# Optimization experiments

Measured on AMD Instinct MI355X. Metric: run time of the kernel, lower is better.

## Reference

```python
import jax, jax.numpy as jnp
import numpy as np

B, T, H = 4, 4096, 1024


def setup_inputs() -> dict:
    key = jax.random.key(0)
    ks = jax.random.split(key, 10)
    W_STD = 0.02  # small init keeps the WKV denominator well-conditioned
    inp = {
        "x": jax.random.normal(ks[0], (B, T, H), dtype=jnp.float32),
        "time_decay": jnp.exp(-jax.random.uniform(ks[1], (H,), minval=0.5, maxval=1.5)),
        "time_mix_key": jax.random.uniform(ks[2], (H,)),
        "time_mix_value": jax.random.uniform(ks[3], (H,)),
        "time_mix_receptance": jax.random.uniform(ks[4], (H,)),
        "W_receptance": jax.random.normal(ks[5], (H, H)) * W_STD,
        "W_key": jax.random.normal(ks[6], (H, H)) * W_STD,
        "W_value": jax.random.normal(ks[7], (H, H)) * W_STD,
        "W_out": jax.random.normal(ks[8], (H, H)) * W_STD,
        "b_out": jax.random.normal(ks[9], (H,)) * W_STD,
    }
    return inp


def reference(x, time_decay, time_mix_key, time_mix_value, time_mix_receptance,
              W_receptance, W_key, W_value, W_out, b_out):
    # time_shift: shifted[:, t] = x[:, t-1], shifted[:, 0] = 0
    shifted = jnp.pad(x, ((0, 0), (1, 0), (0, 0)))[:, :-1]
    xs = x + shifted  # original applies SAME mix to x and shifted
    k = (xs * time_mix_key) @ W_key.T          # [B,T,H]
    v = (xs * time_mix_value) @ W_value.T      # [B,T,H]
    r = jax.nn.sigmoid((xs * time_mix_receptance) @ W_receptance.T)

    def step(carry, kv):
        num, den = carry                       # [B,H] each
        ck, cv = kv                            # [B,H]
        out = (num + time_decay * ck * den) / (den + time_decay * ck)
        ek = jnp.exp(ck)
        return (time_decay * num + ek * cv, time_decay * den + ek), out

    init = (jnp.ones_like(k[:, 0]), jnp.ones_like(k[:, 0]))
    kT = jnp.swapaxes(k, 0, 1)  # [T,B,H]
    vT = jnp.swapaxes(v, 0, 1)
    _, outT = jax.lax.scan(step, init, (kT, vT))
    out = jnp.swapaxes(outT, 0, 1)             # [B,T,H]
    return (r * out) @ W_out.T + b_out
```

## Files before the change

### kernel.cpp

```cpp
#include <hip/hip_runtime.h>

#define H_DIM 1024
#define T_DIM 4096
#define B_DIM 4
#define M_DIM (B_DIM * T_DIM)
#define SCAN_C 64
#define SCAN_W 48

typedef __attribute__((ext_vector_type(8))) short short8;
typedef __attribute__((ext_vector_type(4))) float f32x4;
typedef _Float16 half8 __attribute__((ext_vector_type(8)));

__device__ __forceinline__ unsigned short f2h(float f) {
  _Float16 h = (_Float16)f;
  return __builtin_bit_cast(unsigned short, h);
}
__device__ __forceinline__ float h2f(unsigned short u) {
  return (float)__builtin_bit_cast(_Float16, u);
}

__device__ __forceinline__ double fast_exp64(double x) {
  const double L2E = 1.4426950408889634074;
  const double LN2 = 0.69314718055994530942;
  double z = x * L2E;
  double n = rint(z);
  double y = (z - n) * LN2;
  double p = 2.7557319223985890653e-6;
  p = fma(p, y, 2.4801587301587301566e-5);
  p = fma(p, y, 1.9841269841269841253e-4);
  p = fma(p, y, 1.3888888888888889419e-3);
  p = fma(p, y, 8.3333333333333332177e-3);
  p = fma(p, y, 4.1666666666666664354e-2);
  p = fma(p, y, 1.6666666666666665741e-1);
  p = fma(p, y, 0.5);
  p = fma(p, y, 1.0);
  p = fma(p, y, 1.0);
  long long bits = ((long long)(1023 + (int)n)) << 52;
  return p * __longlong_as_double(bits);
}

__global__ void xs_split_kernel(const float* __restrict__ x,
                                unsigned short* __restrict__ xs1,
                                unsigned short* __restrict__ xs2,
                                int n4) {
  int i = blockIdx.x * blockDim.x + threadIdx.x;
  const int HV = H_DIM / 4;
  if (i >= n4) return;
  int m = i / HV;
  int t = m & (T_DIM - 1);
  float4 cur = reinterpret_cast<const float4*>(x)[i];
  float4 prev = make_float4(0.f, 0.f, 0.f, 0.f);
  if (t > 0) prev = reinterpret_cast<const float4*>(x)[i - HV];
  float s[4] = {cur.x + prev.x, cur.y + prev.y, cur.z + prev.z, cur.w + prev.w};
  unsigned short a1[4], a2[4];
#pragma unroll
  for (int q = 0; q < 4; ++q) {
    unsigned short h1 = f2h(s[q]);
    a1[q] = h1;
    a2[q] = f2h((s[q] - h2f(h1)) * 2048.0f);
  }
  reinterpret_cast<ushort4*>(xs1)[i] = make_ushort4(a1[0], a1[1], a1[2], a1[3]);
  reinterpret_cast<ushort4*>(xs2)[i] = make_ushort4(a2[0], a2[1], a2[2], a2[3]);
}

__global__ void wprep_kernel(const float* __restrict__ Wrec, const float* __restrict__ Wkey,
                             const float* __restrict__ Wval, const float* __restrict__ Wout,
                             const float* __restrict__ tmk, const float* __restrict__ tmv,
                             const float* __restrict__ tmr,
                             unsigned short* __restrict__ WK1H, unsigned short* __restrict__ WK2H,
                             unsigned short* __restrict__ WVRH,
                             unsigned short* __restrict__ WOH) {
  int i = blockIdx.x * blockDim.x + threadIdx.x;
  if (i >= H_DIM * H_DIM) return;
  int j = i & (H_DIM - 1);
  float wk = Wkey[i] * tmk[j];
  unsigned short k1 = f2h(wk);
  WK1H[i] = k1;
  WK2H[i] = f2h((wk - h2f(k1)) * 2048.0f);
  WVRH[i] = f2h(Wval[i] * tmv[j]);
  WVRH[H_DIM * H_DIM + i] = f2h(Wrec[i] * tmr[j]);
  WOH[i] = f2h(Wout[i]);
}

#define GBAR() do { asm volatile("" ::: "memory"); __builtin_amdgcn_sched_barrier(0); \
                    __builtin_amdgcn_s_barrier(); \
                    __builtin_amdgcn_sched_barrier(0); asm volatile("" ::: "memory"); } while (0)
#define WAIT_VM6() asm volatile("s_waitcnt vmcnt(6)" ::: "memory")
#define WAIT_VM0() asm volatile("s_waitcnt vmcnt(0)" ::: "memory")

__device__ __forceinline__ f32x4 mma_h(short8 a, short8 b, f32x4 c) {
  return __builtin_amdgcn_mfma_f32_16x16x32_f16(
      __builtin_bit_cast(half8, a), __builtin_bit_cast(half8, b), c, 0, 0, 0);
}
__device__ __forceinline__ f32x4 mma_hh(half8 a, short8 b, f32x4 c) {
  return __builtin_amdgcn_mfma_f32_16x16x32_f16(a, __builtin_bit_cast(half8, b), c, 0, 0, 0);
}

__device__ __forceinline__ void stage_A32(const unsigned short* base, int rowoff, int kt,
                                          unsigned sbase, int wid, int lane,
                                          unsigned char* smem) {
#pragma unroll
  for (int i = 0; i < 2; ++i) {
    int row = wid * 32 + i * 16 + (lane >> 2);
    int col8 = (lane & 3) ^ ((row >> 1) & 3);
    const unsigned short* src = base + (size_t)(rowoff + row) * 1024 + kt * 32 + col8 * 8;
    __builtin_amdgcn_global_load_lds(
        (const __attribute__((address_space(1))) void*)src,
        (__attribute__((address_space(3))) void*)(smem + sbase + wid * 2048 + i * 1024), 16, 0, 0);
  }
}
__device__ __forceinline__ void stage_B32(const unsigned short* base, int coloff, int kt,
                                          unsigned sbase, int wid, int lane,
                                          unsigned char* smem) {
  int row = wid * 16 + (lane >> 2);
  int col8 = (lane & 3) ^ ((row >> 1) & 3);
  const unsigned short* src = base + (size_t)(coloff + row) * 1024 + kt * 32 + col8 * 8;
  __builtin_amdgcn_global_load_lds(
      (const __attribute__((address_space(1))) void*)src,
      (__attribute__((address_space(3))) void*)(smem + sbase + wid * 1024), 16, 0, 0);
}
__device__ __forceinline__ short8 frag_ld2(const unsigned char* smem, unsigned rbase,
                                           int row, int kg) {
  return *reinterpret_cast<const short8*>(smem + rbase + row * 64 + ((kg ^ ((row >> 1) & 3)) * 16));
}

__global__ __launch_bounds__(512, 2) void gemm_k_kernel(
    const unsigned short* __restrict__ A1, const unsigned short* __restrict__ A2,
    const unsigned short* __restrict__ B1, const unsigned short* __restrict__ B2,
    float* __restrict__ C) {
  __shared__ __attribute__((aligned(16))) unsigned char smem[147456];
  const int tid = threadIdx.x;
  const int wid = tid >> 6;
  const int lane = tid & 63;
  const int wm = wid >> 2;
  const int wn = wid & 3;
  const int frow = lane & 15;
  const int kg = lane >> 4;
  const int nwg = gridDim.x * gridDim.y;
  const int wg = blockIdx.y * gridDim.x + blockIdx.x;
  const int swz = (wg & 7) * (nwg >> 3) + (wg >> 3);
  const int brow = (swz / gridDim.x) << 8;
  const int bcol = (swz % gridDim.x) << 7;

  f32x4 acc0[8][2], acc1[8][2];
#pragma unroll
  for (int f = 0; f < 8; ++f)
#pragma unroll
    for (int c = 0; c < 2; ++c) {
      acc0[f][c] = (f32x4){0.f, 0.f, 0.f, 0.f};
      acc1[f][c] = (f32x4){0.f, 0.f, 0.f, 0.f};
    }

  const int NT = 32;
#pragma unroll
  for (int t0 = 0; t0 < 2; ++t0) {
    unsigned sb = t0 * 49152u;
    stage_A32(A1, brow, t0, sb + 0u, wid, lane, smem);
    stage_A32(A2, brow, t0, sb + 16384u, wid, lane, smem);
    stage_B32(B1, bcol, t0, sb + 32768u, wid, lane, smem);
    stage_B32(B2, bcol, t0, sb + 40960u, wid, lane, smem);
  }
  WAIT_VM6();
  GBAR();

  for (int t = 0; t < NT; ++t) {
    unsigned sb = (unsigned)(t % 3) * 49152u;
    unsigned st = (unsigned)((t + 2) % 3) * 49152u;
    const bool stg = (t + 2 < NT);
    short8 a1[8], a2[8], b1[2], b2[2];
#pragma unroll
    for (int f = 0; f < 8; ++f) a1[f] = frag_ld2(smem, sb, wm * 128 + f * 16 + frow, kg);
#pragma unroll
    for (int c = 0; c < 2; ++c) b1[c] = frag_ld2(smem, sb + 32768u, wn * 32 + c * 16 + frow, kg);
    if (stg) stage_A32(A1, brow, t + 2, st + 0u, wid, lane, smem);
    GBAR();
    __builtin_amdgcn_s_setprio(1);
#pragma unroll
    for (int f = 0; f < 8; ++f)
#pragma unroll
      for (int c = 0; c < 2; ++c)
        acc0[f][c] = mma_h(a1[f], b1[c], acc0[f][c]);
    __builtin_amdgcn_s_setprio(0);
    GBAR();
#pragma unroll
    for (int c = 0; c < 2; ++c) b2[c] = frag_ld2(smem, sb + 40960u, wn * 32 + c * 16 + frow, kg);
    if (stg) stage_A32(A2, brow, t + 2, st + 16384u, wid, lane, smem);
    GBAR();
    __builtin_amdgcn_s_setprio(1);
#pragma unroll
    for (int f = 0; f < 8; ++f)
#pragma unroll
      for (int c = 0; c < 2; ++c)
        acc1[f][c] = mma_h(a1[f], b2[c], acc1[f][c]);
    __builtin_amdgcn_s_setprio(0);
    GBAR();
#pragma unroll
    for (int f = 0; f < 8; ++f) a2[f] = frag_ld2(smem, sb + 16384u, wm * 128 + f * 16 + frow, kg);
    if (stg) {
      stage_B32(B1, bcol, t + 2, st + 32768u, wid, lane, smem);
      stage_B32(B2, bcol, t + 2, st + 40960u, wid, lane, smem);
    }
    GBAR();
    __builtin_amdgcn_s_setprio(1);
#pragma unroll
    for (int f = 0; f < 8; ++f)
#pragma unroll
      for (int c = 0; c < 2; ++c)
        acc1[f][c] = mma_h(a2[f], b1[c], acc1[f][c]);
    __builtin_amdgcn_s_setprio(0);
    GBAR();
    WAIT_VM6();
    GBAR();
    __builtin_amdgcn_s_setprio(1);
#pragma unroll
    for (int f = 0; f < 8; ++f) {
      half8 ad = __builtin_bit_cast(half8, a2[f]) * (_Float16)0.00048828125f;
#pragma unroll
      for (int c = 0; c < 2; ++c)
        acc1[f][c] = mma_hh(ad, b2[c], acc1[f][c]);
    }
    __builtin_amdgcn_s_setprio(0);
    GBAR();
  }
  WAIT_VM0();

#pragma unroll
  for (int f = 0; f < 8; ++f) {
    int r0 = brow + wm * 128 + f * 16 + kg * 4;
#pragma unroll
    for (int c = 0; c < 2; ++c) {
      int cc = bcol + wn * 32 + c * 16 + frow;
#pragma unroll
      for (int q = 0; q < 4; ++q)
        C[(size_t)(r0 + q) * H_DIM + cc] =
            fmaf(0.00048828125f, acc1[f][c][q], acc0[f][c][q]);
    }
  }
}

struct GemmPasses {
  const unsigned short* A[2];
  const unsigned short* B[2];
  int n;
};

__device__ __forceinline__ void stage_half(const unsigned short* base, int rowoff,
                                           int ktp, int kk, int slot,
                                           int wid, int lane, unsigned char* smem) {
#pragma unroll
  for (int i = 0; i < 2; ++i) {
    int row = wid * 32 + i * 16 + (lane >> 2);
    int kcol8 = (lane & 3) ^ ((row >> 1) & 3);
    const unsigned short* src = base + (size_t)(rowoff + row) * 1024
                                + ktp * 64 + kk * 32 + kcol8 * 8;
    unsigned int doff = (unsigned int)(slot * 16384 + wid * 2048 + i * 1024);
    __builtin_amdgcn_global_load_lds(
        (const __attribute__((address_space(1))) void*)src,
        (__attribute__((address_space(3))) void*)(smem + doff), 16, 0, 0);
  }
}
__device__ __forceinline__ short8 frag_ld(const unsigned char* smem, int slot, int row, int kg) {
  int byte = slot * 16384 + row * 64 + ((kg ^ ((row >> 1) & 3)) * 16);
  return *reinterpret_cast<const short8*>(smem + byte);
}

__global__ __launch_bounds__(512, 2) void gemm256_kernel(GemmPasses P, void* __restrict__ Cout,
                                                         int N, int NT,
                                                         const float* __restrict__ bias,
                                                         int omode) {
  __shared__ __attribute__((aligned(16))) unsigned char smem[131072];
  const int tid = threadIdx.x;
  const int wid = tid >> 6;
  const int lane = tid & 63;
  const int wm = wid >> 2;
  const int wn = wid & 3;
  const int frow = lane & 15;
  const int kg = lane >> 4;
  const int nwg = gridDim.x * gridDim.y;
  const int wg = blockIdx.y * gridDim.x + blockIdx.x;
  const int swz = (wg & 7) * (nwg >> 3) + (wg >> 3);
  const int brow = (swz / gridDim.x) << 8;
  const int bcol = (swz % gridDim.x) << 8;

  f32x4 acc[8][4];
#pragma unroll
  for (int f = 0; f < 8; ++f)
#pragma unroll
    for (int c = 0; c < 4; ++c)
      acc[f][c] = (f32x4){0.f, 0.f, 0.f, 0.f};

  const unsigned short* Ag = P.A[0];
  const unsigned short* Bg = P.B[0];
  stage_half(Ag, brow, 0, 0, 0, wid, lane, smem);
  stage_half(Bg, bcol, 0, 0, 1, wid, lane, smem);
  stage_half(Ag, brow, 0, 1, 2, wid, lane, smem);
  stage_half(Bg, bcol, 0, 1, 3, wid, lane, smem);
  stage_half(Ag, brow, 1, 0, 4, wid, lane, smem);
  stage_half(Bg, bcol, 1, 0, 5, wid, lane, smem);
  stage_half(Ag, brow, 1, 1, 6, wid, lane, smem);
  WAIT_VM6();
  GBAR();

  for (int t = 0; t < NT; ++t) {
    const int cur4 = (t & 1) * 4;
    const int nxt4 = cur4 ^ 4;
    const unsigned short* Agp = P.A[(t >> 4) >= P.n ? P.n - 1 : (t >> 4)];
    const unsigned short* Bgp = P.B[(t >> 4) >= P.n ? P.n - 1 : (t >> 4)];
    short8 a[4], b[4];
#pragma unroll
    for (int f = 0; f < 4; ++f) a[f] = frag_ld(smem, cur4 + 0, wm * 128 + f * 16 + frow, kg);
#pragma unroll
    for (int c = 0; c < 4; ++c) b[c] = frag_ld(smem, cur4 + 1, wn * 64 + c * 16 + frow, kg);
    if (t + 1 < NT) {
      int ts = t + 1;
      stage_half(P.B[(ts >> 4)], bcol, ts & 15, 1, nxt4 + 3, wid, lane, smem);
    }
    GBAR();
    __builtin_amdgcn_s_setprio(1);
#pragma unroll
    for (int f = 0; f < 4; ++f)
#pragma unroll
      for (int c = 0; c < 4; ++c)
        acc[f][c] = mma_h(a[f], b[c], acc[f][c]);
    __builtin_amdgcn_s_setprio(0);
    GBAR();
#pragma unroll
    for (int f = 0; f < 4; ++f) a[f] = frag_ld(smem, cur4 + 0, wm * 128 + (f + 4) * 16 + frow, kg);
    if (t + 2 < NT) {
      int ts = t + 2;
      stage_half(P.A[(ts >> 4)], brow, ts & 15, 0, cur4 + 0, wid, lane, smem);
    }
    GBAR();
    __builtin_amdgcn_s_setprio(1);
#pragma unroll
    for (int f = 0; f < 4; ++f)
#pragma unroll
      for (int c = 0; c < 4; ++c)
        acc[f + 4][c] = mma_h(a[f], b[c], acc[f + 4][c]);
    __builtin_amdgcn_s_setprio(0);
    GBAR();
#pragma unroll
    for (int f = 0; f < 4; ++f) a[f] = frag_ld(smem, cur4 + 2, wm * 128 + f * 16 + frow, kg);
#pragma unroll
    for (int c = 0; c < 4; ++c) b[c] = frag_ld(smem, cur4 + 3, wn * 64 + c * 16 + frow, kg);
    if (t + 2 < NT) {
      int ts = t + 2;
      stage_half(P.B[(ts >> 4)], bcol, ts & 15, 0, cur4 + 1, wid, lane, smem);
    }
    GBAR();
    __builtin_amdgcn_s_setprio(1);
#pragma unroll
    for (int f = 0; f < 4; ++f)
#pragma unroll
      for (int c = 0; c < 4; ++c)
        acc[f][c] = mma_h(a[f], b[c], acc[f][c]);
    __builtin_amdgcn_s_setprio(0);
    GBAR();
#pragma unroll
    for (int f = 0; f < 4; ++f) a[f] = frag_ld(smem, cur4 + 2, wm * 128 + (f + 4) * 16 + frow, kg);
    if (t + 2 < NT) {
      int ts = t + 2;
      stage_half(P.A[(ts >> 4)], brow, ts & 15, 1, cur4 + 2, wid, lane, smem);
    }
    WAIT_VM6();
    GBAR();
    __builtin_amdgcn_s_setprio(1);
#pragma unroll
    for (int f = 0; f < 4; ++f)
#pragma unroll
      for (int c = 0; c < 4; ++c)
        acc[f + 4][c] = mma_h(a[f], b[c], acc[f + 4][c]);
    __builtin_amdgcn_s_setprio(0);
    GBAR();
  }
  WAIT_VM0();

#pragma unroll
  for (int f = 0; f < 8; ++f) {
    int r0 = brow + wm * 128 + f * 16 + kg * 4;
#pragma unroll
    for (int c = 0; c < 4; ++c) {
      int cc = bcol + wn * 64 + c * 16 + frow;
      if (omode == 0) {
        float bb = bias ? bias[cc] : 0.f;
        float* C = (float*)Cout;
#pragma unroll
        for (int q = 0; q < 4; ++q)
          C[(size_t)(r0 + q) * N + cc] = acc[f][c][q] + bb;
      } else {
        unsigned short* C = (unsigned short*)Cout;
#pragma unroll
        for (int q = 0; q < 4; ++q)
          C[(size_t)(r0 + q) * N + cc] = f2h(acc[f][c][q]);
      }
    }
  }
}

__global__ void wkv_scan_kernel(const float* __restrict__ kbuf,
                                const unsigned short* __restrict__ vrbuf,
                                const float* __restrict__ tdec,
                                unsigned short* __restrict__ rwh) {
  const int h = blockIdx.x * 64 + threadIdx.x;
  const int chunk = blockIdx.y;
  const int b = blockIdx.z;
  const int t0 = chunk * SCAN_C;
  const int tstart = (chunk == 0) ? 0 : (t0 - SCAN_W);
  const int tend = t0 + SCAN_C;
  double num, den;
  if (chunk == 0) { num = 1.0; den = 1.0; } else { num = 0.0; den = 0.0; }
  const double w = (double)tdec[h];
  size_t ik = ((size_t)b * T_DIM + tstart) * H_DIM + h;
  size_t iv = ((size_t)b * T_DIM + tstart) * 2048 + h;
  float kc = kbuf[ik];
  unsigned short vc = vrbuf[iv];
  unsigned short rc = vrbuf[iv + 1024];
  for (int t = tstart; t < tend; ++t) {
    int adv = (t + 1 < tend) ? 1 : 0;
    float kn = kbuf[ik + adv * H_DIM];
    unsigned short vn = vrbuf[iv + adv * 2048];
    unsigned short rn = vrbuf[iv + adv * 2048 + 1024];
    double ck = (double)kc;
    if (t >= t0) {
      double p = w * ck;
      double A = fma(p, den, num);
      double Bd = den + p;
      float outf = (float)A / (float)Bd;
      float rr = 1.0f / (1.0f + __expf(-h2f(rc)));
      rwh[ik] = f2h(rr * outf);
    }
    double ek = fast_exp64(ck);
    num = fma(w, num, ek * (double)h2f(vc));
    den = fma(w, den, ek);
    kc = kn; vc = vn; rc = rn;
    ik += H_DIM; iv += 2048;
  }
}

static inline void run_gemm256(const GemmPasses& P, void* C, int Mrows, int N,
                               const float* bias, int omode, hipStream_t stream) {
  gemm256_kernel<<<dim3(N / 256, Mrows / 256), dim3(512), 0, stream>>>(
      P, C, N, P.n * 16, bias, omode);
}

extern "C" void kernel_launch(void* const* d_in, const int* in_sizes, int n_in,
                              void* d_out, int out_size, void* d_ws, size_t ws_size,
                              hipStream_t stream) {
  const float* x    = (const float*)d_in[0];
  const float* tdec = (const float*)d_in[1];
  const float* tmk  = (const float*)d_in[2];
  const float* tmv  = (const float*)d_in[3];
  const float* tmr  = (const float*)d_in[4];
  const float* Wrec = (const float*)d_in[5];
  const float* Wkey = (const float*)d_in[6];
  const float* Wval = (const float*)d_in[7];
  const float* Wout = (const float*)d_in[8];
  const float* bout = (const float*)d_in[9];
  float* out = (float*)d_out;
  unsigned char* ws = (unsigned char*)d_ws;

  const size_t W2 = (size_t)H_DIM * H_DIM * 2;
  const size_t BF_FULL = (size_t)M_DIM * H_DIM * 2;
  const size_t NEED = 2 * BF_FULL + 2 * BF_FULL + 5 * W2;
  if (ws_size < NEED) return;

  size_t off = 0;
  unsigned short* XS1H = (unsigned short*)(ws + off); off += BF_FULL;
  unsigned short* XS2H = (unsigned short*)(ws + off); off += BF_FULL;
  unsigned short* VR   = (unsigned short*)(ws + off); off += 2 * BF_FULL;
  unsigned short* WK1H = (unsigned short*)(ws + off); off += W2;
  unsigned short* WK2H = (unsigned short*)(ws + off); off += W2;
  unsigned short* WVRH = (unsigned short*)(ws + off); off += 2 * W2;
  unsigned short* WOH  = (unsigned short*)(ws + off); off += W2;

  wprep_kernel<<<dim3(H_DIM * H_DIM / 256), dim3(256), 0, stream>>>(
      Wrec, Wkey, Wval, Wout, tmk, tmv, tmr, WK1H, WK2H, WVRH, WOH);

  int n4 = M_DIM * (H_DIM / 4);
  xs_split_kernel<<<dim3(n4 / 256), dim3(256), 0, stream>>>(x, XS1H, XS2H, n4);

  GemmPasses Pvr;
  Pvr.n = 1;
  Pvr.A[0] = XS1H; Pvr.B[0] = WVRH; Pvr.A[1] = XS1H; Pvr.B[1] = WVRH;
  run_gemm256(Pvr, VR, M_DIM, 2 * H_DIM, nullptr, 2, stream);

  gemm_k_kernel<<<dim3(H_DIM / 128, M_DIM / 256), dim3(512), 0, stream>>>(
      XS1H, XS2H, WK1H, WK2H, out);

  unsigned short* RWH = XS1H;
  wkv_scan_kernel<<<dim3(H_DIM / 64, T_DIM / SCAN_C, B_DIM), dim3(64), 0, stream>>>(
      out, VR, tdec, RWH);

  GemmPasses Po;
  Po.n = 1;
  Po.A[0] = RWH; Po.B[0] = WOH; Po.A[1] = RWH; Po.B[1] = WOH;
  run_gemm256(Po, out, M_DIM, H_DIM, bout, 0, stream);
}
```

Baseline: 338.2 us.

## Merge K and VR projection GEMMs into one launch and retile K GEMM

```diff
diff --git a/kernel.cpp b/kernel.cpp
--- a/kernel.cpp
+++ b/kernel.cpp
@@ -96,9 +96,19 @@
   return __builtin_amdgcn_mfma_f32_16x16x32_f16(a, __builtin_bit_cast(half8, b), c, 0, 0, 0);
 }
 
-__device__ __forceinline__ void stage_A32(const unsigned short* base, int rowoff, int kt,
-                                          unsigned sbase, int wid, int lane,
-                                          unsigned char* smem) {
+__device__ __forceinline__ void stage_r128(const unsigned short* base, int rowoff, int kt,
+                                           unsigned dst, int wid, int lane,
+                                           unsigned char* smem) {
+  int row = wid * 16 + (lane >> 2);
+  int col8 = (lane & 3) ^ ((row >> 1) & 3);
+  const unsigned short* src = base + (size_t)(rowoff + row) * 1024 + kt * 32 + col8 * 8;
+  __builtin_amdgcn_global_load_lds(
+      (const __attribute__((address_space(1))) void*)src,
+      (__attribute__((address_space(3))) void*)(smem + dst + wid * 1024), 16, 0, 0);
+}
+__device__ __forceinline__ void stage_r256(const unsigned short* base, int rowoff, int kt,
+                                           unsigned dst, int wid, int lane,
+                                           unsigned char* smem) {
 #pragma unroll
   for (int i = 0; i < 2; ++i) {
     int row = wid * 32 + i * 16 + (lane >> 2);
@@ -106,29 +116,19 @@
     const unsigned short* src = base + (size_t)(rowoff + row) * 1024 + kt * 32 + col8 * 8;
     __builtin_amdgcn_global_load_lds(
         (const __attribute__((address_space(1))) void*)src,
-        (__attribute__((address_space(3))) void*)(smem + sbase + wid * 2048 + i * 1024), 16, 0, 0);
-  }
-}
-__device__ __forceinline__ void stage_B32(const unsigned short* base, int coloff, int kt,
-                                          unsigned sbase, int wid, int lane,
-                                          unsigned char* smem) {
-  int row = wid * 16 + (lane >> 2);
-  int col8 = (lane & 3) ^ ((row >> 1) & 3);
-  const unsigned short* src = base + (size_t)(coloff + row) * 1024 + kt * 32 + col8 * 8;
-  __builtin_amdgcn_global_load_lds(
-      (const __attribute__((address_space(1))) void*)src,
-      (__attribute__((address_space(3))) void*)(smem + sbase + wid * 1024), 16, 0, 0);
+        (__attribute__((address_space(3))) void*)(smem + dst + wid * 2048 + i * 1024), 16, 0, 0);
+  }
 }
 __device__ __forceinline__ short8 frag_ld2(const unsigned char* smem, unsigned rbase,
                                            int row, int kg) {
   return *reinterpret_cast<const short8*>(smem + rbase + row * 64 + ((kg ^ ((row >> 1) & 3)) * 16));
 }
 
-__global__ __launch_bounds__(512, 2) void gemm_k_kernel(
-    const unsigned short* __restrict__ A1, const unsigned short* __restrict__ A2,
-    const unsigned short* __restrict__ B1, const unsigned short* __restrict__ B2,
-    float* __restrict__ C) {
-  __shared__ __attribute__((aligned(16))) unsigned char smem[147456];
+__device__ void gemm_k_body(const unsigned short* __restrict__ A1,
+                            const unsigned short* __restrict__ A2,
+                            const unsigned short* __restrict__ B1,
+                            const unsigned short* __restrict__ B2,
+                            float* __restrict__ C, int bid, unsigned char* smem) {
   const int tid = threadIdx.x;
   const int wid = tid >> 6;
   const int lane = tid & 63;
@@ -136,17 +136,15 @@
   const int wn = wid & 3;
   const int frow = lane & 15;
   const int kg = lane >> 4;
-  const int nwg = gridDim.x * gridDim.y;
-  const int wg = blockIdx.y * gridDim.x + blockIdx.x;
-  const int swz = (wg & 7) * (nwg >> 3) + (wg >> 3);
-  const int brow = (swz / gridDim.x) << 8;
-  const int bcol = (swz % gridDim.x) << 7;
-
-  f32x4 acc0[8][2], acc1[8][2];
-#pragma unroll
-  for (int f = 0; f < 8; ++f)
-#pragma unroll
-    for (int c = 0; c < 2; ++c) {
+  const int swz = (bid & 7) * 64 + (bid >> 3);
+  const int brow = (swz >> 2) << 7;
+  const int bcol = (swz & 3) << 8;
+
+  f32x4 acc0[4][4], acc1[4][4];
+#pragma unroll
+  for (int f = 0; f < 4; ++f)
+#pragma unroll
+    for (int c = 0; c < 4; ++c) {
       acc0[f][c] = (f32x4){0.f, 0.f, 0.f, 0.f};
       acc1[f][c] = (f32x4){0.f, 0.f, 0.f, 0.f};
     }
@@ -155,10 +153,10 @@
 #pragma unroll
   for (int t0 = 0; t0 < 2; ++t0) {
     unsigned sb = t0 * 49152u;
-    stage_A32(A1, brow, t0, sb + 0u, wid, lane, smem);
-    stage_A32(A2, brow, t0, sb + 16384u, wid, lane, smem);
-    stage_B32(B1, bcol, t0, sb + 32768u, wid, lane, smem);
-    stage_B32(B2, bcol, t0, sb + 40960u, wid, lane, smem);
+    stage_r128(A1, brow, t0, sb + 0u, wid, lane, smem);
+    stage_r128(A2, brow, t0, sb + 8192u, wid, lane, smem);
+    stage_r256(B1, bcol, t0, sb + 16384u, wid, lane, smem);
+    stage_r256(B2, bcol, t0, sb + 32768u, wid, lane, smem);
   }
   WAIT_VM6();
   GBAR();
@@ -167,56 +165,50 @@
     unsigned sb = (unsigned)(t % 3) * 49152u;
     unsigned st = (unsigned)((t + 2) % 3) * 49152u;
     const bool stg = (t + 2 < NT);
-    short8 a1[8], a2[8], b1[2], b2[2];
-#pragma unroll
-    for (int f = 0; f < 8; ++f) a1[f] = frag_ld2(smem, sb, wm * 128 + f * 16 + frow, kg);
-#pragma unroll
-    for (int c = 0; c < 2; ++c) b1[c] = frag_ld2(smem, sb + 32768u, wn * 32 + c * 16 + frow, kg);
-    if (stg) stage_A32(A1, brow, t + 2, st + 0u, wid, lane, smem);
-    GBAR();
-    __builtin_amdgcn_s_setprio(1);
-#pragma unroll
-    for (int f = 0; f < 8; ++f)
-#pragma unroll
-      for (int c = 0; c < 2; ++c)
+    short8 a1[4], a2[4], b1[4], b2[4];
+#pragma unroll
+    for (int f = 0; f < 4; ++f) a1[f] = frag_ld2(smem, sb + 0u, wm * 64 + f * 16 + frow, kg);
+#pragma unroll
+    for (int c = 0; c < 4; ++c) b1[c] = frag_ld2(smem, sb + 16384u, wn * 64 + c * 16 + frow, kg);
+#pragma unroll
+    for (int c = 0; c < 4; ++c) b2[c] = frag_ld2(smem, sb + 32768u, wn * 64 + c * 16 + frow, kg);
+    if (stg) {
+      stage_r128(A1, brow, t + 2, st + 0u, wid, lane, smem);
+      stage_r128(A2, brow, t + 2, st + 8192u, wid, lane, smem);
+    }
+    GBAR();
+    __builtin_amdgcn_s_setprio(1);
+#pragma unroll
+    for (int f = 0; f < 4; ++f)
+#pragma unroll
+      for (int c = 0; c < 4; ++c)
         acc0[f][c] = mma_h(a1[f], b1[c], acc0[f][c]);
-    __builtin_amdgcn_s_setprio(0);
-    GBAR();
-#pragma unroll
-    for (int c = 0; c < 2; ++c) b2[c] = frag_ld2(smem, sb + 40960u, wn * 32 + c * 16 + frow, kg);
-    if (stg) stage_A32(A2, brow, t + 2, st + 16384u, wid, lane, smem);
-    GBAR();
-    __builtin_amdgcn_s_setprio(1);
-#pragma unroll
-    for (int f = 0; f < 8; ++f)
-#pragma unroll
-      for (int c = 0; c < 2; ++c)
+#pragma unroll
+    for (int f = 0; f < 4; ++f)
+#pragma unroll
+      for (int c = 0; c < 4; ++c)
         acc1[f][c] = mma_h(a1[f], b2[c], acc1[f][c]);
     __builtin_amdgcn_s_setprio(0);
     GBAR();
 #pragma unroll
-    for (int f = 0; f < 8; ++f) a2[f] = frag_ld2(smem, sb + 16384u, wm * 128 + f * 16 + frow, kg);
+    for (int f = 0; f < 4; ++f) a2[f] = frag_ld2(smem, sb + 8192u, wm * 64 + f * 16 + frow, kg);
     if (stg) {
-      stage_B32(B1, bcol, t + 2, st + 32768u, wid, lane, smem);
-      stage_B32(B2, bcol, t + 2, st + 40960u, wid, lane, smem);
-    }
-    GBAR();
-    __builtin_amdgcn_s_setprio(1);
-#pragma unroll
-    for (int f = 0; f < 8; ++f)
-#pragma unroll
-      for (int c = 0; c < 2; ++c)
+      stage_r256(B1, bcol, t + 2, st + 16384u, wid, lane, smem);
+      stage_r256(B2, bcol, t + 2, st + 32768u, wid, lane, smem);
+    }
+    WAIT_VM6();
+    GBAR();
+    __builtin_amdgcn_s_setprio(1);
+#pragma unroll
+    for (int f = 0; f < 4; ++f)
+#pragma unroll
+      for (int c = 0; c < 4; ++c)
         acc1[f][c] = mma_h(a2[f], b1[c], acc1[f][c]);
-    __builtin_amdgcn_s_setprio(0);
-    GBAR();
-    WAIT_VM6();
-    GBAR();
-    __builtin_amdgcn_s_setprio(1);
-#pragma unroll
-    for (int f = 0; f < 8; ++f) {
+#pragma unroll
+    for (int f = 0; f < 4; ++f) {
       half8 ad = __builtin_bit_cast(half8, a2[f]) * (_Float16)0.00048828125f;
 #pragma unroll
-      for (int c = 0; c < 2; ++c)
+      for (int c = 0; c < 4; ++c)
         acc1[f][c] = mma_hh(ad, b2[c], acc1[f][c]);
     }
     __builtin_amdgcn_s_setprio(0);
@@ -225,11 +217,11 @@
   WAIT_VM0();
 
 #pragma unroll
-  for (int f = 0; f < 8; ++f) {
-    int r0 = brow + wm * 128 + f * 16 + kg * 4;
-#pragma unroll
-    for (int c = 0; c < 2; ++c) {
-      int cc = bcol + wn * 32 + c * 16 + frow;
+  for (int f = 0; f < 4; ++f) {
+    int r0 = brow + wm * 64 + f * 16 + kg * 4;
+#pragma unroll
+    for (int c = 0; c < 4; ++c) {
+      int cc = bcol + wn * 64 + c * 16 + frow;
 #pragma unroll
       for (int q = 0; q < 4; ++q)
         C[(size_t)(r0 + q) * H_DIM + cc] =
@@ -237,12 +229,6 @@
     }
   }
 }
-
-struct GemmPasses {
-  const unsigned short* A[2];
-  const unsigned short* B[2];
-  int n;
-};
 
 __device__ __forceinline__ void stage_half(const unsigned short* base, int rowoff,
                                            int ktp, int kk, int slot,
@@ -264,10 +250,129 @@
   return *reinterpret_cast<const short8*>(smem + byte);
 }
 
-__global__ __launch_bounds__(512, 2) void gemm256_kernel(GemmPasses P, void* __restrict__ Cout,
-                                                         int N, int NT,
-                                                         const float* __restrict__ bias,
-                                                         int omode) {
+__device__ void gemm_vr_body(const unsigned short* __restrict__ Ag,
+                             const unsigned short* __restrict__ Bg,
+                             unsigned short* __restrict__ C, int bid,
+                             unsigned char* smem) {
+  const int tid = threadIdx.x;
+  const int wid = tid >> 6;
+  const int lane = tid & 63;
+  const int wm = wid >> 2;
+  const int wn = wid & 3;
+  const int frow = lane & 15;
+  const int kg = lane >> 4;
+  const int swz = (bid & 7) * 64 + (bid >> 3);
+  const int brow = (swz >> 3) << 8;
+  const int bcol = (swz & 7) << 8;
+
+  f32x4 acc[8][4];
+#pragma unroll
+  for (int f = 0; f < 8; ++f)
+#pragma unroll
+    for (int c = 0; c < 4; ++c)
+      acc[f][c] = (f32x4){0.f, 0.f, 0.f, 0.f};
+
+  const int NT = 16;
+  stage_half(Ag, brow, 0, 0, 0, wid, lane, smem);
+  stage_half(Bg, bcol, 0, 0, 1, wid, lane, smem);
+  stage_half(Ag, brow, 0, 1, 2, wid, lane, smem);
+  stage_half(Bg, bcol, 0, 1, 3, wid, lane, smem);
+  stage_half(Ag, brow, 1, 0, 4, wid, lane, smem);
+  stage_half(Bg, bcol, 1, 0, 5, wid, lane, smem);
+  stage_half(Ag, brow, 1, 1, 6, wid, lane, smem);
+  WAIT_VM6();
+  GBAR();
+
+  for (int t = 0; t < NT; ++t) {
+    const int cur4 = (t & 1) * 4;
+    const int nxt4 = cur4 ^ 4;
+    short8 a[4], b[4];
+#pragma unroll
+    for (int f = 0; f < 4; ++f) a[f] = frag_ld(smem, cur4 + 0, wm * 128 + f * 16 + frow, kg);
+#pragma unroll
+    for (int c = 0; c < 4; ++c) b[c] = frag_ld(smem, cur4 + 1, wn * 64 + c * 16 + frow, kg);
+    if (t + 1 < NT) stage_half(Bg, bcol, t + 1, 1, nxt4 + 3, wid, lane, smem);
+    GBAR();
+    __builtin_amdgcn_s_setprio(1);
+#pragma unroll
+    for (int f = 0; f < 4; ++f)
+#pragma unroll
+      for (int c = 0; c < 4; ++c)
+        acc[f][c] = mma_h(a[f], b[c], acc[f][c]);
+    __builtin_amdgcn_s_setprio(0);
+    GBAR();
+#pragma unroll
+    for (int f = 0; f < 4; ++f) a[f] = frag_ld(smem, cur4 + 0, wm * 128 + (f + 4) * 16 + frow, kg);
+    if (t + 2 < NT) stage_half(Ag, brow, t + 2, 0, cur4 + 0, wid, lane, smem);
+    GBAR();
+    __builtin_amdgcn_s_setprio(1);
+#pragma unroll
+    for (int f = 0; f < 4; ++f)
+#pragma unroll
+      for (int c = 0; c < 4; ++c)
+        acc[f + 4][c] = mma_h(a[f], b[c], acc[f + 4][c]);
+    __builtin_amdgcn_s_setprio(0);
+    GBAR();
+#pragma unroll
+    for (int f = 0; f < 4; ++f) a[f] = frag_ld(smem, cur4 + 2, wm * 128 + f * 16 + frow, kg);
+#pragma unroll
+    for (int c = 0; c < 4; ++c) b[c] = frag_ld(smem, cur4 + 3, wn * 64 + c * 16 + frow, kg);
+    if (t + 2 < NT) stage_half(Bg, bcol, t + 2, 0, cur4 + 1, wid, lane, smem);
+    GBAR();
+    __builtin_amdgcn_s_setprio(1);
+#pragma unroll
+    for (int f = 0; f < 4; ++f)
+#pragma unroll
+      for (int c = 0; c < 4; ++c)
+        acc[f][c] = mma_h(a[f], b[c], acc[f][c]);
+    __builtin_amdgcn_s_setprio(0);
+    GBAR();
+#pragma unroll
+    for (int f = 0; f < 4; ++f) a[f] = frag_ld(smem, cur4 + 2, wm * 128 + (f + 4) * 16 + frow, kg);
+    if (t + 2 < NT) stage_half(Ag, brow, t + 2, 1, cur4 + 2, wid, lane, smem);
+    WAIT_VM6();
+    GBAR();
+    __builtin_amdgcn_s_setprio(1);
+#pragma unroll
+    for (int f = 0; f < 4; ++f)
+#pragma unroll
+      for (int c = 0; c < 4; ++c)
+        acc[f + 4][c] = mma_h(a[f], b[c], acc[f + 4][c]);
+    __builtin_amdgcn_s_setprio(0);
+    GBAR();
+  }
+  WAIT_VM0();
+
+#pragma unroll
+  for (int f = 0; f < 8; ++f) {
+    int r0 = brow + wm * 128 + f * 16 + kg * 4;
+#pragma unroll
+    for (int c = 0; c < 4; ++c) {
+      int cc = bcol + wn * 64 + c * 16 + frow;
+#pragma unroll
+      for (int q = 0; q < 4; ++q)
+        C[(size_t)(r0 + q) * 2048 + cc] = f2h(acc[f][c][q]);
+    }
+  }
+}
+
+__global__ __launch_bounds__(512, 2) void front_kernel(
+    const unsigned short* __restrict__ XS1, const unsigned short* __restrict__ XS2,
+    const unsigned short* __restrict__ WK1, const unsigned short* __restrict__ WK2,
+    const unsigned short* __restrict__ WVR,
+    float* __restrict__ Ck, unsigned short* __restrict__ Cvr) {
+  __shared__ __attribute__((aligned(16))) unsigned char smem[147456];
+  int bid = blockIdx.x;
+  if (bid < 512)
+    gemm_k_body(XS1, XS2, WK1, WK2, Ck, bid, smem);
+  else
+    gemm_vr_body(XS1, WVR, Cvr, bid - 512, smem);
+}
+
+__global__ __launch_bounds__(512, 2) void gemm_o_kernel(const unsigned short* __restrict__ Ag,
+                                                        const unsigned short* __restrict__ Bg,
+                                                        float* __restrict__ C,
+                                                        const float* __restrict__ bias) {
   __shared__ __attribute__((aligned(16))) unsigned char smem[131072];
   const int tid = threadIdx.x;
   const int wid = tid >> 6;
@@ -289,8 +394,7 @@
     for (int c = 0; c < 4; ++c)
       acc[f][c] = (f32x4){0.f, 0.f, 0.f, 0.f};
 
-  const unsigned short* Ag = P.A[0];
-  const unsigned short* Bg = P.B[0];
+  const int NT = 16;
   stage_half(Ag, brow, 0, 0, 0, wid, lane, smem);
   stage_half(Bg, bcol, 0, 0, 1, wid, lane, smem);
   stage_half(Ag, brow, 0, 1, 2, wid, lane, smem);
@@ -304,17 +408,12 @@
   for (int t = 0; t < NT; ++t) {
     const int cur4 = (t & 1) * 4;
     const int nxt4 = cur4 ^ 4;
-    const unsigned short* Agp = P.A[(t >> 4) >= P.n ? P.n - 1 : (t >> 4)];
-    const unsigned short* Bgp = P.B[(t >> 4) >= P.n ? P.n - 1 : (t >> 4)];
     short8 a[4], b[4];
 #pragma unroll
     for (int f = 0; f < 4; ++f) a[f] = frag_ld(smem, cur4 + 0, wm * 128 + f * 16 + frow, kg);
 #pragma unroll
     for (int c = 0; c < 4; ++c) b[c] = frag_ld(smem, cur4 + 1, wn * 64 + c * 16 + frow, kg);
-    if (t + 1 < NT) {
-      int ts = t + 1;
-      stage_half(P.B[(ts >> 4)], bcol, ts & 15, 1, nxt4 + 3, wid, lane, smem);
-    }
+    if (t + 1 < NT) stage_half(Bg, bcol, t + 1, 1, nxt4 + 3, wid, lane, smem);
     GBAR();
     __builtin_amdgcn_s_setprio(1);
 #pragma unroll
@@ -326,10 +425,7 @@
     GBAR();
 #pragma unroll
     for (int f = 0; f < 4; ++f) a[f] = frag_ld(smem, cur4 + 0, wm * 128 + (f + 4) * 16 + frow, kg);
-    if (t + 2 < NT) {
-      int ts = t + 2;
-      stage_half(P.A[(ts >> 4)], brow, ts & 15, 0, cur4 + 0, wid, lane, smem);
-    }
+    if (t + 2 < NT) stage_half(Ag, brow, t + 2, 0, cur4 + 0, wid, lane, smem);
     GBAR();
     __builtin_amdgcn_s_setprio(1);
 #pragma unroll
@@ -343,10 +439,7 @@
     for (int f = 0; f < 4; ++f) a[f] = frag_ld(smem, cur4 + 2, wm * 128 + f * 16 + frow, kg);
 #pragma unroll
     for (int c = 0; c < 4; ++c) b[c] = frag_ld(smem, cur4 + 3, wn * 64 + c * 16 + frow, kg);
-    if (t + 2 < NT) {
-      int ts = t + 2;
-      stage_half(P.B[(ts >> 4)], bcol, ts & 15, 0, cur4 + 1, wid, lane, smem);
-    }
+    if (t + 2 < NT) stage_half(Bg, bcol, t + 2, 0, cur4 + 1, wid, lane, smem);
     GBAR();
     __builtin_amdgcn_s_setprio(1);
 #pragma unroll
@@ -358,10 +451,7 @@
     GBAR();
 #pragma unroll
     for (int f = 0; f < 4; ++f) a[f] = frag_ld(smem, cur4 + 2, wm * 128 + (f + 4) * 16 + frow, kg);
-    if (t + 2 < NT) {
-      int ts = t + 2;
-      stage_half(P.A[(ts >> 4)], brow, ts & 15, 1, cur4 + 2, wid, lane, smem);
-    }
+    if (t + 2 < NT) stage_half(Ag, brow, t + 2, 1, cur4 + 2, wid, lane, smem);
     WAIT_VM6();
     GBAR();
     __builtin_amdgcn_s_setprio(1);
@@ -381,18 +471,10 @@
 #pragma unroll
     for (int c = 0; c < 4; ++c) {
       int cc = bcol + wn * 64 + c * 16 + frow;
-      if (omode == 0) {
-        float bb = bias ? bias[cc] : 0.f;
-        float* C = (float*)Cout;
-#pragma unroll
-        for (int q = 0; q < 4; ++q)
-          C[(size_t)(r0 + q) * N + cc] = acc[f][c][q] + bb;
-      } else {
-        unsigned short* C = (unsigned short*)Cout;
-#pragma unroll
-        for (int q = 0; q < 4; ++q)
-          C[(size_t)(r0 + q) * N + cc] = f2h(acc[f][c][q]);
-      }
+      float bb = bias[cc];
+#pragma unroll
+      for (int q = 0; q < 4; ++q)
+        C[(size_t)(r0 + q) * H_DIM + cc] = acc[f][c][q] + bb;
     }
   }
 }
@@ -437,12 +519,6 @@
   }
 }
 
-static inline void run_gemm256(const GemmPasses& P, void* C, int Mrows, int N,
-                               const float* bias, int omode, hipStream_t stream) {
-  gemm256_kernel<<<dim3(N / 256, Mrows / 256), dim3(512), 0, stream>>>(
-      P, C, N, P.n * 16, bias, omode);
-}
-
 extern "C" void kernel_launch(void* const* d_in, const int* in_sizes, int n_in,
                               void* d_out, int out_size, void* d_ws, size_t ws_size,
                               hipStream_t stream) {
@@ -479,20 +555,13 @@
   int n4 = M_DIM * (H_DIM / 4);
   xs_split_kernel<<<dim3(n4 / 256), dim3(256), 0, stream>>>(x, XS1H, XS2H, n4);
 
-  GemmPasses Pvr;
-  Pvr.n = 1;
-  Pvr.A[0] = XS1H; Pvr.B[0] = WVRH; Pvr.A[1] = XS1H; Pvr.B[1] = WVRH;
-  run_gemm256(Pvr, VR, M_DIM, 2 * H_DIM, nullptr, 2, stream);
-
-  gemm_k_kernel<<<dim3(H_DIM / 128, M_DIM / 256), dim3(512), 0, stream>>>(
-      XS1H, XS2H, WK1H, WK2H, out);
+  front_kernel<<<dim3(1024), dim3(512), 0, stream>>>(
+      XS1H, XS2H, WK1H, WK2H, WVRH, out, VR);
 
   unsigned short* RWH = XS1H;
   wkv_scan_kernel<<<dim3(H_DIM / 64, T_DIM / SCAN_C, B_DIM), dim3(64), 0, stream>>>(
       out, VR, tdec, RWH);
 
-  GemmPasses Po;
-  Po.n = 1;
-  Po.A[0] = RWH; Po.B[0] = WOH; Po.A[1] = RWH; Po.B[1] = WOH;
-  run_gemm256(Po, out, M_DIM, H_DIM, bout, 0, stream);
-}
+  gemm_o_kernel<<<dim3(H_DIM / 256, M_DIM / 256), dim3(512), 0, stream>>>(
+      RWH, WOH, out, bout);
+}
```

Result: faster. 322.2 us (-4.7%).
